# Kernel optimization log

Measured on AMD Instinct MI355X. Metric: run time of the kernel, lower is better.

## Reference

```python
import jax, jax.numpy as jnp
import numpy as np

# Sizes: B graphs of N nodes each, K nearest neighbours, D=feat_dim=nhid, C=pos_dim
B, N, K, D, C = 4, 1024, 128, 32, 2
L = 3                     # number of EGNN conv layers
E_IN = 2 * D + 1          # edge MLP input: feats_i | feats_j | rel_dist (edge_dim=0, fourier=0)
E_H = 2 * E_IN            # edge MLP hidden


def _lin(key, fan_in, fan_out):
    kw, kb = jax.random.split(key)
    w = jax.random.normal(kw, (fan_in, fan_out), jnp.float32) / np.sqrt(fan_in)
    b = jax.random.normal(kb, (fan_out,), jnp.float32) * 0.01
    return w, b


def _stack(key, fan_in, fan_out):
    ws, bs = zip(*[_lin(k, fan_in, fan_out) for k in jax.random.split(key, L)])
    return jnp.stack(ws), jnp.stack(bs)


def setup_inputs() -> dict:
    key = jax.random.key(0)
    ks = jax.random.split(key, 10)
    feat_ = jax.random.normal(ks[0], (B * N, D), jnp.float32)
    coor_ = jax.random.normal(ks[1], (B * N, C), jnp.float32)
    batch = jnp.full((B,), N, dtype=jnp.int32)   # per-graph node counts (equal-size graphs)
    embed_w, embed_b = _lin(ks[2], D, D)         # embed: Linear(feat_dim, nhid)
    e1_w, e1_b = _stack(ks[3], E_IN, E_H)        # edge MLP
    e2_w, e2_b = _stack(ks[4], E_H, D)           # -> m_dim = nhid
    gate_w, gate_b = _stack(ks[5], D, 1)         # soft_edges gate
    c1_w, c1_b = _stack(ks[6], D, 4 * D)         # coors MLP
    c2_w, c2_b = _stack(ks[7], 4 * D, 1)
    n1_w, n1_b = _stack(ks[8], 2 * D, 2 * D)     # node MLP
    n2_w, n2_b = _stack(ks[9], 2 * D, D)
    coors_scale = jnp.full((L, 1), 1e-2, jnp.float32)  # CoorsNorm scale (init 1e-2)
    return dict(feat_=feat_, coor_=coor_, batch=batch, embed_w=embed_w, embed_b=embed_b,
                e1_w=e1_w, e1_b=e1_b, e2_w=e2_w, e2_b=e2_b, gate_w=gate_w, gate_b=gate_b,
                c1_w=c1_w, c1_b=c1_b, c2_w=c2_w, c2_b=c2_b, n1_w=n1_w, n1_b=n1_b,
                n2_w=n2_w, n2_b=n2_b, coors_scale=coors_scale)


def _lrelu(x):
    return jax.nn.leaky_relu(x, 0.1)


def _gather(x, idx):
    # x: [B, n, d], idx: [B, n, k] -> [B, n, k, d]
    return jax.vmap(lambda xb, ib: xb[ib])(x, idx)


def _egnn_layer(feats, coors, p):
    (e1_w, e1_b, e2_w, e2_b, gate_w, gate_b, c1_w, c1_b, c2_w, c2_b,
     n1_w, n1_b, n2_w, n2_b, scale) = p
    # pairwise squared distances; k smallest (self included, valid_radius=inf)
    diff = coors[:, :, None, :] - coors[:, None, :, :]      # [B,n,n,C]
    dist = jnp.sum(diff * diff, axis=-1)                    # [B,n,n]
    neg_d, idx = jax.lax.top_k(-dist, K)                    # k nearest
    rel_dist = -neg_d[..., None]                            # [B,n,K,1]
    rel_coors = coors[:, :, None, :] - _gather(coors, idx)  # [B,n,K,C]
    feats_j = _gather(feats, idx)                           # [B,n,K,D]
    feats_i = jnp.broadcast_to(feats[:, :, None, :], feats_j.shape)
    edge_in = jnp.concatenate([feats_i, feats_j, rel_dist], axis=-1)  # [B,n,K,E_IN]
    # edge MLP: Lin -> act -> Lin -> act ; soft edge gate
    m = _lrelu(_lrelu(edge_in @ e1_w + e1_b) @ e2_w + e2_b)            # [B,n,K,D]
    m = m * jax.nn.sigmoid(m @ gate_w + gate_b)
    # coordinate update: coors_mlp -> scalar weights; CoorsNorm on rel coords
    cw = (_lrelu(m @ c1_w + c1_b) @ c2_w + c2_b)[..., 0]               # [B,n,K]
    norm = jnp.maximum(jnp.linalg.norm(rel_coors, axis=-1, keepdims=True), 1e-8)
    rel_n = rel_coors / norm * scale
    coors_out = jnp.einsum('bik,bikc->bic', cw, rel_n) + coors
    # feature update: sum-pool messages, node MLP with residual
    m_i = jnp.sum(m, axis=2)                                           # [B,n,D]
    node_in = jnp.concatenate([feats, m_i], axis=-1)
    feats_out = _lrelu(node_in @ n1_w + n1_b) @ n2_w + n2_b + feats
    return feats_out, coors_out


def reference(feat_, coor_, batch, embed_w, embed_b, e1_w, e1_b, e2_w, e2_b,
              gate_w, gate_b, c1_w, c1_b, c2_w, c2_b, n1_w, n1_b, n2_w, n2_b,
              coors_scale):
    # embed MLP (dropout is identity at p=0 / eval), then batch equal-size graphs
    feats = _lrelu(feat_ @ embed_w + embed_b).reshape(B, N, D)
    coors = coor_.reshape(B, N, C)
    for l in range(L):
        p = (e1_w[l], e1_b[l], e2_w[l], e2_b[l], gate_w[l], gate_b[l],
             c1_w[l], c1_b[l], c2_w[l], c2_b[l], n1_w[l], n1_b[l],
             n2_w[l], n2_b[l], coors_scale[l])
        feats, coors = _egnn_layer(feats, coors, p)
    return feats.reshape(B * N, D)
```

## Files before the change

### kernel.cpp

```cpp
#include <hip/hip_runtime.h>
#include <hip/hip_bf16.h>
#include <math.h>

#define BB 4
#define NN 1024
#define KK 128
#define DD 32
#define LL 3
#define EH 130
#define EHP 132

typedef float f32x4 __attribute__((ext_vector_type(4)));
typedef short s16x8 __attribute__((ext_vector_type(8)));

__device__ __forceinline__ float lrelu(float x) { return fmaxf(x, 0.1f * x); }

__device__ __forceinline__ unsigned pk2(float a, float b) {
    __hip_bfloat162 h = __float22bfloat162_rn(float2{a, b});
    return *(unsigned*)&h;
}
__device__ __forceinline__ unsigned short bf16_hu(float v) {
    return (unsigned short)((__float_as_uint(v) + 0x8000u) >> 16);
}
__device__ __forceinline__ unsigned short bf16_rne(float v) {
    unsigned u = __float_as_uint(v);
    return (unsigned short)((u + 0x7fffu + ((u >> 16) & 1u)) >> 16);
}

__global__ void embed_kernel(const float* __restrict__ feat,
                             const float* __restrict__ w,
                             const float* __restrict__ b,
                             float* __restrict__ out) {
    int t = blockIdx.x * blockDim.x + threadIdx.x;
    if (t >= BB * NN * DD) return;
    int n = t >> 5, o = t & 31;
    const float* f = feat + n * DD;
    float a = b[o];
#pragma unroll
    for (int k = 0; k < DD; k++) a = fmaf(f[k], w[k * DD + o], a);
    out[t] = lrelu(a);
}

__global__ void frag_kernel(const float* __restrict__ e2w, const float* __restrict__ c1w,
                            unsigned short* __restrict__ e2f, unsigned short* __restrict__ c1f) {
    int t = blockIdx.x * 256 + threadIdx.x;
    if (t < LL * 4 * 2 * 512) {
        int jj = t & 7, lane = (t >> 3) & 63, nt = (t >> 9) & 1, c = (t >> 10) & 3, l = t >> 12;
        int k = 32 * c + (lane >> 4) * 8 + jj;
        int n = nt * 16 + (lane & 15);
        e2f[t] = bf16_rne(e2w[(size_t)l * EH * DD + k * DD + n]);
    } else {
        int u = t - LL * 4 * 2 * 512;
        if (u < LL * 8 * 512) {
            int jj = u & 7, lane = (u >> 3) & 63, nt = (u >> 9) & 7, l = u >> 12;
            int k = (lane >> 4) * 8 + jj;
            int n = nt * 16 + (lane & 15);
            c1f[u] = bf16_rne(c1w[(size_t)l * DD * 128 + k * 128 + n]);
        }
    }
}

__global__ void pre_kernel(const float* __restrict__ feats,
                           const float* __restrict__ e1w,
                           const float* __restrict__ e1b,
                           float* __restrict__ HI, float* __restrict__ HJ) {
    int t = blockIdx.x * blockDim.x + threadIdx.x;
    if (t >= BB * NN * EHP) return;
    int n = t / EHP, o = t % EHP;
    if (o >= EH) { HI[t] = 0.f; HJ[t] = 0.f; return; }
    const float* f = feats + n * DD;
    float a = e1b[o], c = 0.f;
#pragma unroll
    for (int k = 0; k < DD; k++) a = fmaf(f[k], e1w[k * EH + o], a);
#pragma unroll
    for (int k = 0; k < DD; k++) c = fmaf(f[k], e1w[(DD + k) * EH + o], c);
    HI[t] = a;
    HJ[t] = c;
}

__global__ __launch_bounds__(256) void knn_kernel(const float* __restrict__ coors,
                                                  int* __restrict__ nbr) {
    const int node = blockIdx.x;
    const int b = node >> 10, i = node & (NN - 1);
    const int t = threadIdx.x;

    __shared__ unsigned dkey[NN];
    __shared__ unsigned h1[256];
    __shared__ unsigned eqi[NN];
    __shared__ unsigned bsel[2];
    __shared__ unsigned scnt[2];

    const float2* cb = (const float2*)(coors + (size_t)b * NN * 2);
    const float2 ci = cb[i];

#pragma unroll
    for (int c = 0; c < 4; c++) {
        int j = t + c * 256;
        float2 cj = cb[j];
        float dx = ci.x - cj.x, dy = ci.y - cj.y;
        float d = __fadd_rn(__fmul_rn(dx, dx), __fmul_rn(dy, dy));
        dkey[j] = __float_as_uint(d);
    }
    if (t < 2) scnt[t] = 0;
    __syncthreads();

    unsigned maskSo = 0u, valSo = 0u;
    unsigned R_rem = KK - 1;
    for (int pass = 0; pass < 4; pass++) {
        const int shift = 24 - 8 * pass;
        h1[t] = 0;
        __syncthreads();
#pragma unroll
        for (int c = 0; c < 4; c++) {
            unsigned k = dkey[t + c * 256];
            if ((k & maskSo) == valSo) atomicAdd(&h1[(k >> shift) & 0xFFu], 1u);
        }
        __syncthreads();
        unsigned mine = h1[t];
        for (int off = 1; off < 256; off <<= 1) {
            unsigned v = h1[t];
            if (t >= off) v += h1[t - off];
            __syncthreads();
            h1[t] = v;
            __syncthreads();
        }
        if (R_rem < h1[t] && R_rem >= h1[t] - mine) {
            bsel[0] = (unsigned)t;
            bsel[1] = h1[t] - mine;
        }
        __syncthreads();
        valSo |= bsel[0] << shift;
        maskSo |= 0xFFu << shift;
        R_rem -= bsel[1];
        __syncthreads();
    }
    const unsigned dstar = valSo;

#pragma unroll
    for (int c = 0; c < 4; c++) {
        int j = t + c * 256;
        unsigned k = dkey[j];
        if (k < dstar) {
            unsigned slot = atomicAdd(&scnt[0], 1u);
            nbr[(size_t)node * KK + slot] = j;
        } else if (k == dstar) {
            unsigned slot = atomicAdd(&scnt[1], 1u);
            eqi[slot] = (unsigned)j;
        }
    }
    __syncthreads();
    const unsigned base = scnt[0];
    const int E = (int)scnt[1];
    const int need = KK - (int)base;
    if (E == need) {
        for (int c = t; c < E; c += 256)
            nbr[(size_t)node * KK + base + c] = (int)eqi[c];
    } else {
        for (int r = 0; r < need; r++) {
            unsigned best = 0xFFFFFFFFu;
            for (int c = t; c < E; c += 256) best = min(best, eqi[c]);
            h1[t] = best;
            __syncthreads();
            for (int off = 128; off >= 1; off >>= 1) {
                if (t < off) h1[t] = min(h1[t], h1[t + off]);
                __syncthreads();
            }
            unsigned win = h1[0];
            __syncthreads();
            if (t == 0) nbr[(size_t)node * KK + base + r] = (int)win;
            for (int c = t; c < E; c += 256)
                if (eqi[c] == win) eqi[c] = 0xFFFFFFFFu;
            __syncthreads();
        }
    }
}

__global__ __launch_bounds__(128) void layer_kernel(
    const float* __restrict__ feats_in, const float* __restrict__ coors_in,
    const int*   __restrict__ nbr,
    const float* __restrict__ HI, const float* __restrict__ HJ,
    const float* __restrict__ w65,
    const float* __restrict__ e2w,
    const float* __restrict__ e2b,
    const unsigned short* __restrict__ e2f,
    const unsigned short* __restrict__ c1f,
    const float* __restrict__ gw, const float* __restrict__ gb,
    const float* __restrict__ c1b, const float* __restrict__ c2w, const float* __restrict__ c2b,
    const float* __restrict__ n1w, const float* __restrict__ n1b,
    const float* __restrict__ n2w, const float* __restrict__ n2b,
    const float* __restrict__ scale,
    float* __restrict__ feats_out, float* __restrict__ coors_out) {
    const int node = blockIdx.x;
    const int b = node >> 10;
    const int t = threadIdx.x;
    const int lane = t & 63, wid = t >> 6;
    const int ln = lane & 15, q = lane >> 4;
    const int rowbase = wid * 64;

    __shared__ __align__(16) float shi[EHP];
    __shared__ __align__(16) float sw65[EHP];
    __shared__ __align__(16) unsigned short smA[2 * 64 * 32];
    __shared__ float sx0[128], sx1[128], su[128], sv[128];
    __shared__ float sgw[DD], se2b[DD], sfi[DD];
    __shared__ float sc1b[128], sc2w[128];
    __shared__ float redm[2][DD], redc[2][2];
    __shared__ float sni[2 * DD], shd[2 * DD];

    for (int u = t; u < EHP; u += 128) {
        shi[u] = HI[(size_t)node * EHP + u];
        sw65[u] = (u < EH) ? w65[u] : 0.f;
    }
    if (t < DD) { sfi[t] = feats_in[node * DD + t]; sgw[t] = gw[t]; se2b[t] = e2b[t]; }
    sc1b[t] = c1b[t];
    sc2w[t] = c2w[t];
    __syncthreads();

    const float cix = coors_in[node * 2], ciy = coors_in[node * 2 + 1];
    const int j = nbr[(size_t)node * KK + t];
    const float2 cj = *(const float2*)(coors_in + ((size_t)(b * NN) + j) * 2);
    const float dx = cix - cj.x, dy = ciy - cj.y;
    const float rd = __fadd_rn(__fmul_rn(dx, dx), __fmul_rn(dy, dy));
    const float nrm = fmaxf(sqrtf(rd), 1e-8f);
    const float s = scale[0] / nrm;
    su[t] = dx * s;
    sv[t] = dy * s;

    {
        const float2 hjt = *(const float2*)(HJ + ((size_t)(b * NN) + j) * EHP + 128);
        sx0[t] = lrelu(shi[128] + hjt.x + rd * sw65[128]);
        sx1[t] = lrelu(shi[129] + hjt.y + rd * sw65[129]);
    }

    const float* hjb[4];
    float rdR[4];
#pragma unroll
    for (int mt = 0; mt < 4; mt++) {
        int jR = __shfl(j, mt * 16 + ln, 64);
        rdR[mt] = __shfl(rd, mt * 16 + ln, 64);
        hjb[mt] = HJ + ((size_t)(b * NN) + jR) * EHP;
    }

    const float4* shi4 = (const float4*)shi;
    const float4* sw4  = (const float4*)sw65;

    const f32x4 zz = {0.f, 0.f, 0.f, 0.f};
    f32x4 accA[4][2];
#pragma unroll
    for (int mt = 0; mt < 4; mt++) { accA[mt][0] = zz; accA[mt][1] = zz; }

#pragma unroll 1
    for (int c = 0; c < 4; c++) {
        s16x8 b0 = *(const s16x8*)(e2f + ((c * 2 + 0) * 64 + lane) * 8);
        s16x8 b1 = *(const s16x8*)(e2f + ((c * 2 + 1) * 64 + lane) * 8);
        const int kb = c * 8 + q * 2;
        const float4 hi0 = shi4[kb], hi1 = shi4[kb + 1];
        const float4 wv0 = sw4[kb],  wv1 = sw4[kb + 1];
#pragma unroll
        for (int mt = 0; mt < 4; mt++) {
            const float4* hjp = (const float4*)(hjb[mt] + c * 32 + q * 8);
            const float4 ha = hjp[0], hb = hjp[1];
            const float r = rdR[mt];
            union { s16x8 v; unsigned u[4]; } A;
            A.u[0] = pk2(lrelu(hi0.x + ha.x + r * wv0.x), lrelu(hi0.y + ha.y + r * wv0.y));
            A.u[1] = pk2(lrelu(hi0.z + ha.z + r * wv0.z), lrelu(hi0.w + ha.w + r * wv0.w));
            A.u[2] = pk2(lrelu(hi1.x + hb.x + r * wv1.x), lrelu(hi1.y + hb.y + r * wv1.y));
            A.u[3] = pk2(lrelu(hi1.z + hb.z + r * wv1.z), lrelu(hi1.w + hb.w + r * wv1.w));
            accA[mt][0] = __builtin_amdgcn_mfma_f32_16x16x32_bf16(A.v, b0, accA[mt][0], 0, 0, 0);
            accA[mt][1] = __builtin_amdgcn_mfma_f32_16x16x32_bf16(A.v, b1, accA[mt][1], 0, 0, 0);
        }
    }

#pragma unroll
    for (int nt = 0; nt < 2; nt++) {
        const int col = nt * 16 + ln;
        const float w128 = e2w[128 * DD + col];
        const float w129 = e2w[129 * DD + col];
        const float bv = se2b[col];
#pragma unroll
        for (int mt = 0; mt < 4; mt++)
#pragma unroll
            for (int r = 0; r < 4; r++) {
                const int row = rowbase + mt * 16 + q * 4 + r;
                accA[mt][nt][r] = lrelu(accA[mt][nt][r] + bv + sx0[row] * w128 + sx1[row] * w129);
            }
    }

    const float gbv = gb[0];
#pragma unroll
    for (int mt = 0; mt < 4; mt++) {
        float p[4];
#pragma unroll
        for (int r = 0; r < 4; r++)
            p[r] = accA[mt][0][r] * sgw[ln] + accA[mt][1][r] * sgw[16 + ln];
#pragma unroll
        for (int off = 1; off <= 8; off <<= 1)
#pragma unroll
            for (int r = 0; r < 4; r++) p[r] += __shfl_xor(p[r], off);
#pragma unroll
        for (int r = 0; r < 4; r++) {
            const float g = 1.f / (1.f + __expf(-(p[r] + gbv)));
            accA[mt][0][r] *= g;
            accA[mt][1][r] *= g;
        }
    }

    float mi0 = 0.f, mi1 = 0.f;
#pragma unroll
    for (int mt = 0; mt < 4; mt++)
#pragma unroll
        for (int r = 0; r < 4; r++) { mi0 += accA[mt][0][r]; mi1 += accA[mt][1][r]; }
    mi0 += __shfl_xor(mi0, 16); mi0 += __shfl_xor(mi0, 32);
    mi1 += __shfl_xor(mi1, 16); mi1 += __shfl_xor(mi1, 32);
    if (lane < 16) { redm[wid][lane] = mi0; redm[wid][16 + lane] = mi1; }

    unsigned short* smw = smA + wid * (64 * 32);
#pragma unroll
    for (int mt = 0; mt < 4; mt++)
#pragma unroll
        for (int nt = 0; nt < 2; nt++)
#pragma unroll
            for (int r = 0; r < 4; r++) {
                const int prow = (r << 4) | (4 * mt + q);
                smw[prow * 32 + nt * 16 + ln] = bf16_hu(accA[mt][nt][r]);
            }

    s16x8 a4[4];
#pragma unroll
    for (int mt = 0; mt < 4; mt++) {
        const int prow = ((ln & 3) << 4) | (4 * mt + (ln >> 2));
        a4[mt] = *(const s16x8*)(smw + prow * 32 + q * 8);
    }

    float cacc[4][4];
#pragma unroll
    for (int mt = 0; mt < 4; mt++)
#pragma unroll
        for (int r = 0; r < 4; r++) cacc[mt][r] = 0.f;

#pragma unroll 1
    for (int g = 0; g < 4; g++) {
        s16x8 bc0 = *(const s16x8*)(c1f + ((2 * g + 0) * 64 + lane) * 8);
        s16x8 bc1 = *(const s16x8*)(c1f + ((2 * g + 1) * 64 + lane) * 8);
        f32x4 c20[4], c21[4];
#pragma unroll
        for (int mt = 0; mt < 4; mt++) {
            c20[mt] = __builtin_amdgcn_mfma_f32_16x16x32_bf16(a4[mt], bc0, zz, 0, 0, 0);
            c21[mt] = __builtin_amdgcn_mfma_f32_16x16x32_bf16(a4[mt], bc1, zz, 0, 0, 0);
        }
#pragma unroll
        for (int h = 0; h < 2; h++) {
            const int col = (2 * g + h) * 16 + ln;
            const float c1bv = sc1b[col], c2wv = sc2w[col];
#pragma unroll
            for (int mt = 0; mt < 4; mt++)
#pragma unroll
                for (int r = 0; r < 4; r++) {
                    const float v = (h ? c21[mt][r] : c20[mt][r]) + c1bv;
                    cacc[mt][r] = fmaf(lrelu(v), c2wv, cacc[mt][r]);
                }
        }
    }
#pragma unroll
    for (int off = 1; off <= 8; off <<= 1)
#pragma unroll
        for (int mt = 0; mt < 4; mt++)
#pragma unroll
            for (int r = 0; r < 4; r++) cacc[mt][r] += __shfl_xor(cacc[mt][r], off);

    const float c2bv = c2b[0];
    float vxp = 0.f, vyp = 0.f;
    if (ln == 0) {
#pragma unroll
        for (int mt = 0; mt < 4; mt++)
#pragma unroll
            for (int r = 0; r < 4; r++) {
                const int row = rowbase + mt * 16 + q * 4 + r;
                const float cw = cacc[mt][r] + c2bv;
                vxp = fmaf(cw, su[row], vxp);
                vyp = fmaf(cw, sv[row], vyp);
            }
    }
    vxp += __shfl_xor(vxp, 16); vxp += __shfl_xor(vxp, 32);
    vyp += __shfl_xor(vyp, 16); vyp += __shfl_xor(vyp, 32);
    if (lane == 0) { redc[wid][0] = vxp; redc[wid][1] = vyp; }

    __syncthreads();
    if (t < DD) {
        sni[t] = sfi[t];
        sni[DD + t] = redm[0][t] + redm[1][t];
    }
    __syncthreads();
    if (t < 2 * DD) {
        float a = n1b[t];
#pragma unroll
        for (int k = 0; k < 2 * DD; k++) a = fmaf(sni[k], n1w[k * 2 * DD + t], a);
        shd[t] = lrelu(a);
    }
    __syncthreads();
    if (t < DD) {
        float a = n2b[t];
#pragma unroll
        for (int o = 0; o < 2 * DD; o++) a = fmaf(shd[o], n2w[o * DD + t], a);
        feats_out[node * DD + t] = a + sfi[t];
    }
    if (t == 0) {
        coors_out[node * 2] = cix + redc[0][0] + redc[1][0];
        coors_out[node * 2 + 1] = ciy + redc[0][1] + redc[1][1];
    }
}

extern "C" void kernel_launch(void* const* d_in, const int* in_sizes, int n_in,
                              void* d_out, int out_size, void* d_ws, size_t ws_size,
                              hipStream_t stream) {
    const float* feat_   = (const float*)d_in[0];
    const float* coor_   = (const float*)d_in[1];
    const float* embed_w = (const float*)d_in[3];
    const float* embed_b = (const float*)d_in[4];
    const float* e1_w    = (const float*)d_in[5];
    const float* e1_b    = (const float*)d_in[6];
    const float* e2_w    = (const float*)d_in[7];
    const float* e2_b    = (const float*)d_in[8];
    const float* gate_w  = (const float*)d_in[9];
    const float* gate_b  = (const float*)d_in[10];
    const float* c1_w    = (const float*)d_in[11];
    const float* c1_b    = (const float*)d_in[12];
    const float* c2_w    = (const float*)d_in[13];
    const float* c2_b    = (const float*)d_in[14];
    const float* n1_w    = (const float*)d_in[15];
    const float* n1_b    = (const float*)d_in[16];
    const float* n2_w    = (const float*)d_in[17];
    const float* n2_b    = (const float*)d_in[18];
    const float* cscale  = (const float*)d_in[19];

    float* ws = (float*)d_ws;
    float* feats_a = ws;               ws += BB * NN * DD;
    float* feats_b = ws;               ws += BB * NN * DD;
    float* coors_a = ws;               ws += BB * NN * 2;
    float* coors_b = ws;               ws += BB * NN * 2;
    float* HI      = ws;               ws += BB * NN * EHP;
    float* HJ      = ws;               ws += BB * NN * EHP;
    unsigned short* e2f = (unsigned short*)ws;
    unsigned short* c1f = e2f + LL * 4096;
    ws += (2 * LL * 4096) / 2;
    int* nbr = (int*)ws;

    embed_kernel<<<(BB * NN * DD + 255) / 256, 256, 0, stream>>>(feat_, embed_w, embed_b, feats_a);
    frag_kernel<<<(2 * LL * 4096 + 255) / 256, 256, 0, stream>>>(e2_w, c1_w, e2f, c1f);

    const float* fin = feats_a;
    const float* cin = coor_;
    float* fouts[LL] = {feats_b, feats_a, (float*)d_out};
    float* couts[LL] = {coors_a, coors_b, coors_a};

    for (int l = 0; l < LL; l++) {
        knn_kernel<<<BB * NN, 256, 0, stream>>>(cin, nbr);
        pre_kernel<<<(BB * NN * EHP + 255) / 256, 256, 0, stream>>>(
            fin, e1_w + (size_t)l * 65 * EH, e1_b + (size_t)l * EH, HI, HJ);
        layer_kernel<<<BB * NN, 128, 0, stream>>>(
            fin, cin, nbr, HI, HJ,
            e1_w + ((size_t)l * 65 + 64) * EH,
            e2_w + (size_t)l * EH * DD,
            e2_b + (size_t)l * DD,
            e2f + (size_t)l * 4096,
            c1f + (size_t)l * 4096,
            gate_w + (size_t)l * DD,
            gate_b + l,
            c1_b + (size_t)l * 128,
            c2_w + (size_t)l * 128,
            c2_b + l,
            n1_w + (size_t)l * 64 * 64,
            n1_b + (size_t)l * 64,
            n2_w + (size_t)l * 64 * 32,
            n2_b + (size_t)l * DD,
            cscale + l,
            fouts[l], couts[l]);
        fin = fouts[l];
        cin = couts[l];
    }
}
```

Before: 391.4 us.

## Merge prep and knn/pre kernels; speed up radix-select with wave scans and early exit

Merges the embed and weight-fragment kernels into one launch, and the knn and per-node edge-MLP precompute into one launch, using blockIdx ranges to pick the role. The knn radix select now keeps distance keys in registers, replaces the shared-memory Hillis-Steele scan with wave shuffles plus per-wave sums, and stops the radix passes once at most 256 candidates remain, then finds the threshold with a direct rank count. This is meant to cut launch overhead, barrier count and shared-memory traffic in the neighbour search. It adds code complexity and an O(c) per-thread rank loop.

```diff
diff --git a/kernel.cpp b/kernel.cpp
--- a/kernel.cpp
+++ b/kernel.cpp
@@ -27,125 +27,155 @@
     return (unsigned short)((u + 0x7fffu + ((u >> 16) & 1u)) >> 16);
 }
 
-__global__ void embed_kernel(const float* __restrict__ feat,
-                             const float* __restrict__ w,
-                             const float* __restrict__ b,
-                             float* __restrict__ out) {
-    int t = blockIdx.x * blockDim.x + threadIdx.x;
-    if (t >= BB * NN * DD) return;
-    int n = t >> 5, o = t & 31;
-    const float* f = feat + n * DD;
-    float a = b[o];
-#pragma unroll
-    for (int k = 0; k < DD; k++) a = fmaf(f[k], w[k * DD + o], a);
-    out[t] = lrelu(a);
-}
-
-__global__ void frag_kernel(const float* __restrict__ e2w, const float* __restrict__ c1w,
-                            unsigned short* __restrict__ e2f, unsigned short* __restrict__ c1f) {
-    int t = blockIdx.x * 256 + threadIdx.x;
-    if (t < LL * 4 * 2 * 512) {
-        int jj = t & 7, lane = (t >> 3) & 63, nt = (t >> 9) & 1, c = (t >> 10) & 3, l = t >> 12;
-        int k = 32 * c + (lane >> 4) * 8 + jj;
-        int n = nt * 16 + (lane & 15);
-        e2f[t] = bf16_rne(e2w[(size_t)l * EH * DD + k * DD + n]);
+__global__ __launch_bounds__(256) void prep_kernel(
+    const float* __restrict__ feat, const float* __restrict__ ew, const float* __restrict__ eb,
+    float* __restrict__ out,
+    const float* __restrict__ e2w, const float* __restrict__ c1w,
+    unsigned short* __restrict__ e2f, unsigned short* __restrict__ c1f) {
+    if (blockIdx.x < 512) {
+        int t = blockIdx.x * 256 + threadIdx.x;
+        if (t >= BB * NN * DD) return;
+        int n = t >> 5, o = t & 31;
+        const float* f = feat + n * DD;
+        float a = eb[o];
+#pragma unroll
+        for (int k = 0; k < DD; k++) a = fmaf(f[k], ew[k * DD + o], a);
+        out[t] = lrelu(a);
     } else {
-        int u = t - LL * 4 * 2 * 512;
-        if (u < LL * 8 * 512) {
-            int jj = u & 7, lane = (u >> 3) & 63, nt = (u >> 9) & 7, l = u >> 12;
-            int k = (lane >> 4) * 8 + jj;
+        int t = (blockIdx.x - 512) * 256 + threadIdx.x;
+        if (t < LL * 4 * 2 * 512) {
+            int jj = t & 7, lane = (t >> 3) & 63, nt = (t >> 9) & 1, c = (t >> 10) & 3, l = t >> 12;
+            int k = 32 * c + (lane >> 4) * 8 + jj;
             int n = nt * 16 + (lane & 15);
-            c1f[u] = bf16_rne(c1w[(size_t)l * DD * 128 + k * 128 + n]);
-        }
-    }
-}
-
-__global__ void pre_kernel(const float* __restrict__ feats,
-                           const float* __restrict__ e1w,
-                           const float* __restrict__ e1b,
-                           float* __restrict__ HI, float* __restrict__ HJ) {
-    int t = blockIdx.x * blockDim.x + threadIdx.x;
-    if (t >= BB * NN * EHP) return;
-    int n = t / EHP, o = t % EHP;
-    if (o >= EH) { HI[t] = 0.f; HJ[t] = 0.f; return; }
-    const float* f = feats + n * DD;
-    float a = e1b[o], c = 0.f;
-#pragma unroll
-    for (int k = 0; k < DD; k++) a = fmaf(f[k], e1w[k * EH + o], a);
-#pragma unroll
-    for (int k = 0; k < DD; k++) c = fmaf(f[k], e1w[(DD + k) * EH + o], c);
-    HI[t] = a;
-    HJ[t] = c;
-}
-
-__global__ __launch_bounds__(256) void knn_kernel(const float* __restrict__ coors,
-                                                  int* __restrict__ nbr) {
+            e2f[t] = bf16_rne(e2w[(size_t)l * EH * DD + k * DD + n]);
+        } else {
+            int u = t - LL * 4 * 2 * 512;
+            if (u < LL * 8 * 512) {
+                int jj = u & 7, lane = (u >> 3) & 63, nt = (u >> 9) & 7, l = u >> 12;
+                int k = (lane >> 4) * 8 + jj;
+                int n = nt * 16 + (lane & 15);
+                c1f[u] = bf16_rne(c1w[(size_t)l * DD * 128 + k * 128 + n]);
+            }
+        }
+    }
+}
+
+__global__ __launch_bounds__(256) void knnpre_kernel(
+    const float* __restrict__ coors, int* __restrict__ nbr,
+    const float* __restrict__ feats, const float* __restrict__ e1w, const float* __restrict__ e1b,
+    float* __restrict__ HI, float* __restrict__ HJ) {
+    if (blockIdx.x >= BB * NN) {
+        int t = (int)(blockIdx.x - BB * NN) * 256 + threadIdx.x;
+        if (t >= BB * NN * EHP) return;
+        int n = t / EHP, o = t % EHP;
+        if (o >= EH) { HI[t] = 0.f; HJ[t] = 0.f; return; }
+        const float* f = feats + n * DD;
+        float a = e1b[o], c = 0.f;
+#pragma unroll
+        for (int k = 0; k < DD; k++) a = fmaf(f[k], e1w[k * EH + o], a);
+#pragma unroll
+        for (int k = 0; k < DD; k++) c = fmaf(f[k], e1w[(DD + k) * EH + o], c);
+        HI[t] = a;
+        HJ[t] = c;
+        return;
+    }
     const int node = blockIdx.x;
     const int b = node >> 10, i = node & (NN - 1);
     const int t = threadIdx.x;
-
-    __shared__ unsigned dkey[NN];
-    __shared__ unsigned h1[256];
-    __shared__ unsigned eqi[NN];
-    __shared__ unsigned bsel[2];
-    __shared__ unsigned scnt[2];
+    const int lane = t & 63, w = t >> 6;
+
+    __shared__ unsigned cand[NN];
+    __shared__ unsigned hh[256];
+    __shared__ unsigned wsum[4];
+    __shared__ unsigned bsel[3];
+    __shared__ unsigned scnt[3];
+    __shared__ unsigned sdstar;
 
     const float2* cb = (const float2*)(coors + (size_t)b * NN * 2);
     const float2 ci = cb[i];
-
+    unsigned k4[4];
 #pragma unroll
     for (int c = 0; c < 4; c++) {
         int j = t + c * 256;
         float2 cj = cb[j];
         float dx = ci.x - cj.x, dy = ci.y - cj.y;
         float d = __fadd_rn(__fmul_rn(dx, dx), __fmul_rn(dy, dy));
-        dkey[j] = __float_as_uint(d);
-    }
-    if (t < 2) scnt[t] = 0;
-    __syncthreads();
+        k4[c] = __float_as_uint(d);
+    }
+    if (t < 3) scnt[t] = 0;
 
     unsigned maskSo = 0u, valSo = 0u;
-    unsigned R_rem = KK - 1;
-    for (int pass = 0; pass < 4; pass++) {
+    unsigned R = KK - 1;
+    unsigned c = NN;
+    for (int pass = 0; pass < 4 && c > 256u; pass++) {
         const int shift = 24 - 8 * pass;
-        h1[t] = 0;
-        __syncthreads();
-#pragma unroll
-        for (int c = 0; c < 4; c++) {
-            unsigned k = dkey[t + c * 256];
-            if ((k & maskSo) == valSo) atomicAdd(&h1[(k >> shift) & 0xFFu], 1u);
-        }
-        __syncthreads();
-        unsigned mine = h1[t];
-        for (int off = 1; off < 256; off <<= 1) {
-            unsigned v = h1[t];
-            if (t >= off) v += h1[t - off];
-            __syncthreads();
-            h1[t] = v;
-            __syncthreads();
-        }
-        if (R_rem < h1[t] && R_rem >= h1[t] - mine) {
-            bsel[0] = (unsigned)t;
-            bsel[1] = h1[t] - mine;
-        }
+        hh[t] = 0;
+        __syncthreads();
+#pragma unroll
+        for (int cc = 0; cc < 4; cc++) {
+            unsigned k = k4[cc];
+            if ((k & maskSo) == valSo) atomicAdd(&hh[(k >> shift) & 255u], 1u);
+        }
+        __syncthreads();
+        const unsigned mine = hh[t];
+        unsigned v = mine;
+#pragma unroll
+        for (int off = 1; off < 64; off <<= 1) {
+            unsigned u = __shfl_up(v, off, 64);
+            if (lane >= off) v += u;
+        }
+        if (lane == 63) wsum[w] = v;
+        __syncthreads();
+        unsigned pre = 0;
+#pragma unroll
+        for (int s = 0; s < 3; s++) if (s < w) pre += wsum[s];
+        const unsigned cum = v + pre;
+        if (R < cum && R >= cum - mine) { bsel[0] = (unsigned)t; bsel[1] = cum - mine; bsel[2] = mine; }
         __syncthreads();
         valSo |= bsel[0] << shift;
-        maskSo |= 0xFFu << shift;
-        R_rem -= bsel[1];
-        __syncthreads();
-    }
-    const unsigned dstar = valSo;
-
-#pragma unroll
-    for (int c = 0; c < 4; c++) {
-        int j = t + c * 256;
-        unsigned k = dkey[j];
+        maskSo |= 255u << shift;
+        R -= bsel[1];
+        c = bsel[2];
+        __syncthreads();
+    }
+
+    unsigned dstar;
+    if (c > 256u) {
+        dstar = valSo;
+    } else {
+#pragma unroll
+        for (int cc = 0; cc < 4; cc++) {
+            unsigned k = k4[cc];
+            if ((k & maskSo) == valSo) {
+                unsigned slot = atomicAdd(&scnt[2], 1u);
+                cand[slot] = k;
+            }
+        }
+        __syncthreads();
+        if (t < (int)c) {
+            const unsigned kt = cand[t];
+            unsigned less = 0, eq = 0;
+            for (unsigned s = 0; s < c; s++) {
+                unsigned ks = cand[s];
+                less += (ks < kt);
+                eq += (ks == kt);
+            }
+            if (less <= R && R < less + eq) sdstar = kt;
+        }
+        __syncthreads();
+        dstar = sdstar;
+    }
+
+#pragma unroll
+    for (int cc = 0; cc < 4; cc++) {
+        int j = t + cc * 256;
+        unsigned k = k4[cc];
         if (k < dstar) {
             unsigned slot = atomicAdd(&scnt[0], 1u);
             nbr[(size_t)node * KK + slot] = j;
         } else if (k == dstar) {
             unsigned slot = atomicAdd(&scnt[1], 1u);
-            eqi[slot] = (unsigned)j;
+            cand[slot] = (unsigned)j;
         }
     }
     __syncthreads();
@@ -153,23 +183,23 @@
     const int E = (int)scnt[1];
     const int need = KK - (int)base;
     if (E == need) {
-        for (int c = t; c < E; c += 256)
-            nbr[(size_t)node * KK + base + c] = (int)eqi[c];
+        for (int cc = t; cc < E; cc += 256)
+            nbr[(size_t)node * KK + base + cc] = (int)cand[cc];
     } else {
         for (int r = 0; r < need; r++) {
             unsigned best = 0xFFFFFFFFu;
-            for (int c = t; c < E; c += 256) best = min(best, eqi[c]);
-            h1[t] = best;
+            for (int cc = t; cc < E; cc += 256) best = min(best, cand[cc]);
+            hh[t] = best;
             __syncthreads();
             for (int off = 128; off >= 1; off >>= 1) {
-                if (t < off) h1[t] = min(h1[t], h1[t + off]);
+                if (t < off) hh[t] = min(hh[t], hh[t + off]);
                 __syncthreads();
             }
-            unsigned win = h1[0];
+            unsigned win = hh[0];
             __syncthreads();
             if (t == 0) nbr[(size_t)node * KK + base + r] = (int)win;
-            for (int c = t; c < E; c += 256)
-                if (eqi[c] == win) eqi[c] = 0xFFFFFFFFu;
+            for (int cc = t; cc < E; cc += 256)
+                if (cand[cc] == win) cand[cc] = 0xFFFFFFFFu;
             __syncthreads();
         }
     }
@@ -444,18 +474,18 @@
     ws += (2 * LL * 4096) / 2;
     int* nbr = (int*)ws;
 
-    embed_kernel<<<(BB * NN * DD + 255) / 256, 256, 0, stream>>>(feat_, embed_w, embed_b, feats_a);
-    frag_kernel<<<(2 * LL * 4096 + 255) / 256, 256, 0, stream>>>(e2_w, c1_w, e2f, c1f);
-
+    prep_kernel<<<512 + 96, 256, 0, stream>>>(feat_, embed_w, embed_b, feats_a,
+                                              e2_w, c1_w, e2f, c1f);
+
+    const int PREB = (BB * NN * EHP + 255) / 256;
     const float* fin = feats_a;
     const float* cin = coor_;
     float* fouts[LL] = {feats_b, feats_a, (float*)d_out};
     float* couts[LL] = {coors_a, coors_b, coors_a};
 
     for (int l = 0; l < LL; l++) {
-        knn_kernel<<<BB * NN, 256, 0, stream>>>(cin, nbr);
-        pre_kernel<<<(BB * NN * EHP + 255) / 256, 256, 0, stream>>>(
-            fin, e1_w + (size_t)l * 65 * EH, e1_b + (size_t)l * EH, HI, HJ);
+        knnpre_kernel<<<BB * NN + PREB, 256, 0, stream>>>(
+            cin, nbr, fin, e1_w + (size_t)l * 65 * EH, e1_b + (size_t)l * EH, HI, HJ);
         layer_kernel<<<BB * NN, 128, 0, stream>>>(
             fin, cin, nbr, HI, HJ,
             e1_w + ((size_t)l * 65 + 64) * EH,
```

Measured after the change: 384.1 us. Within noise of the previous version (-1.9%).
